# Kernel tuning notes

Hardware: AMD Instinct MI355X
Metric: run time of the kernel (lower is better)

The kernel has to match this reference:

```python
import jax, jax.numpy as jnp
import numpy as np

INPUT, HIDDEN, OUTPUT = 512, 1024, 512
B, T = 256, 512

def setup_inputs() -> dict:
    key = jax.random.key(0)
    ks = jax.random.split(key, 15)
    def lin(k, fin, fout):
        bound = 1.0 / np.sqrt(fin)
        kw, kb = jax.random.split(k)
        W = jax.random.uniform(kw, (fout, fin), jnp.float32, -bound, bound)
        b = jax.random.uniform(kb, (fout,), jnp.float32, -bound, bound)
        return W, b
    x = jax.random.normal(ks[0], (B, T, INPUT), jnp.float32)
    Wxr, bxr = lin(ks[1], INPUT, HIDDEN)
    Whr, bhr = lin(ks[2], HIDDEN, HIDDEN)
    Wxc, bxc = lin(ks[3], INPUT, HIDDEN)
    Whc, bhc = lin(ks[4], HIDDEN, HIDDEN)
    Wxz, bxz = lin(ks[5], INPUT, HIDDEN)
    Whz, bhz = lin(ks[6], HIDDEN, HIDDEN)
    Wo, bo = lin(ks[7], HIDDEN, OUTPUT)
    return {"x": x, "Wxr": Wxr, "bxr": bxr, "Whr": Whr, "bhr": bhr,
            "Wxc": Wxc, "bxc": bxc, "Whc": Whc, "bhc": bhc,
            "Wxz": Wxz, "bxz": bxz, "Whz": Whz, "bhz": bhz,
            "Wo": Wo, "bo": bo}

def reference(x, Wxr, bxr, Whr, bhr, Wxc, bxc, Whc, bhc, Wxz, bxz, Whz, bhz, Wo, bo):
    # Precompute all input-to-gate projections in one big GEMM each: [B,T,H]
    xr = jnp.einsum('bti,hi->bth', x, Wxr) + bxr
    xc = jnp.einsum('bti,hi->bth', x, Wxc) + bxc
    xz = jnp.einsum('bti,hi->bth', x, Wxz) + bxz
    # time-major for scan: [T,B,H]
    xs = (xr.transpose(1, 0, 2), xc.transpose(1, 0, 2), xz.transpose(1, 0, 2))

    h0 = jnp.zeros((x.shape[0], Whr.shape[0]), x.dtype)

    def step(h, xt):
        xr_t, xc_t, xz_t = xt
        r = jax.nn.sigmoid(xr_t + h @ Whr.T + bhr)
        c = jnp.tanh(xc_t + r * (h @ Whc.T + bhc))
        z = jax.nn.sigmoid(xz_t + h @ Whz.T + bhz)
        h_new = (1.0 - z) * h + z * c
        return h_new, None

    h_final, _ = jax.lax.scan(step, h0, xs)
    return h_final @ Wo.T + bo
```

## Files before the change

kernel.cpp:

```cpp
#include <hip/hip_runtime.h>

typedef __attribute__((ext_vector_type(8))) short s16x8;
typedef __attribute__((ext_vector_type(4))) float f32x4;

#define SCOPE_AGENT __HIP_MEMORY_SCOPE_AGENT

static __device__ __forceinline__ unsigned short f2bf(float f) {
    unsigned u = __float_as_uint(f);
    u = (u + 0x7fffu + ((u >> 16) & 1u)) >> 16;
    return (unsigned short)u;
}

static __device__ __forceinline__ unsigned ld_sc1(const unsigned* p) {
    return __hip_atomic_load(p, __ATOMIC_RELAXED, SCOPE_AGENT);
}
static __device__ __forceinline__ void st_sc1(unsigned* p, unsigned v) {
    __hip_atomic_store(p, v, __ATOMIC_RELAXED, SCOPE_AGENT);
}

__global__ void k_cast_bf16(const float* __restrict__ src,
                            unsigned short* __restrict__ dst, int n4) {
    int i = blockIdx.x * blockDim.x + threadIdx.x;
    int stride = gridDim.x * blockDim.x;
    for (; i < n4; i += stride) {
        float4 v = reinterpret_cast<const float4*>(src)[i];
        ushort4 o;
        o.x = f2bf(v.x); o.y = f2bf(v.y); o.z = f2bf(v.z); o.w = f2bf(v.w);
        reinterpret_cast<ushort4*>(dst)[i] = o;
    }
}

__global__ __launch_bounds__(256, 1) void k_gru(
    const unsigned short* __restrict__ x16,
    const unsigned short* __restrict__ wh,
    const unsigned short* __restrict__ wx,
    const unsigned short* __restrict__ wo,
    const float* __restrict__ bxr_, const float* __restrict__ bhr_,
    const float* __restrict__ bxc_, const float* __restrict__ bhc_,
    const float* __restrict__ bxz_, const float* __restrict__ bhz_,
    const float* __restrict__ bo_,
    unsigned short* __restrict__ hring,
    unsigned* __restrict__ slots,
    float* __restrict__ out)
{
    extern __shared__ unsigned short lds[];

    const int tid = threadIdx.x;
    const int bid = blockIdx.x;
    const int xcd = bid & 7;
    const int rb  = xcd >> 1;
    const int jt  = ((bid >> 3) << 1) | (xcd & 1);
    const int b0  = rb * 64;
    const int j0  = jt * 16;

    for (int i = 0; i < 36; ++i) {
        int gidx = i * 256 + tid;
        int rr = gidx / 192;
        int gc = gidx - rr * 192;
        int k  = gc << 3;
        int gate = rr >> 4;
        int j = j0 + (rr & 15);
        const unsigned short* src =
            (k < 1024) ? (wh + ((size_t)gate << 20) + ((size_t)j << 10) + k)
                       : (wx + (size_t)gate * 524288 + ((size_t)j << 9) + (k - 1024));
        s16x8 v = *reinterpret_cast<const s16x8*>(src);
        int boff = ((rr * 192 + gc) << 4) ^ ((rr & 15) << 4);
        *reinterpret_cast<s16x8*>(reinterpret_cast<char*>(lds) + boff) = v;
    }
    __syncthreads();

    const int lane = tid & 63;
    const int wv   = tid >> 6;
    const int l15  = lane & 15;
    const int lk   = lane >> 4;

    const int b   = b0 + wv * 16 + l15;
    const int jq  = j0 + lk * 4;
    const int swz = l15 << 4;
    const int rbase0 = (l15)      * 192 + lk;
    const int rbase1 = (16 + l15) * 192 + lk;
    const int rbase2 = (32 + l15) * 192 + lk;

    float bR[4], bZ[4], bCh[4], bCx[4];
#pragma unroll
    for (int e = 0; e < 4; ++e) {
        int j = jq + e;
        bR[e]  = bxr_[j] + bhr_[j];
        bZ[e]  = bxz_[j] + bhz_[j];
        bCh[e] = bhc_[j];
        bCx[e] = bxc_[j];
    }

    float hreg[4] = {0.f, 0.f, 0.f, 0.f};
    char* lb = reinterpret_cast<char*>(lds);
    const unsigned short* xrowbase = x16 + (size_t)b * 262144 + lk * 8;
    unsigned* myflag  = &slots[(rb << 6) + jt];
    unsigned* gflags  = &slots[rb << 6];

    f32x4 xR = {0.f,0.f,0.f,0.f}, xZ = {0.f,0.f,0.f,0.f}, xC = {0.f,0.f,0.f,0.f};
    {
        s16x8 xf[16];
#pragma unroll
        for (int kk = 0; kk < 16; ++kk)
            xf[kk] = *reinterpret_cast<const s16x8*>(xrowbase + kk * 32);
#pragma unroll
        for (int kk = 0; kk < 16; ++kk) {
            s16x8 w0 = *reinterpret_cast<s16x8*>(lb + (((rbase0 + (kk + 32) * 4) << 4) ^ swz));
            s16x8 w1 = *reinterpret_cast<s16x8*>(lb + (((rbase1 + (kk + 32) * 4) << 4) ^ swz));
            s16x8 w2 = *reinterpret_cast<s16x8*>(lb + (((rbase2 + (kk + 32) * 4) << 4) ^ swz));
            xR = __builtin_amdgcn_mfma_f32_16x16x32_bf16(w0, xf[kk], xR, 0, 0, 0);
            xC = __builtin_amdgcn_mfma_f32_16x16x32_bf16(w1, xf[kk], xC, 0, 0, 0);
            xZ = __builtin_amdgcn_mfma_f32_16x16x32_bf16(w2, xf[kk], xZ, 0, 0, 0);
        }
    }

    for (int t = 0; t < 512; ++t) {
        const unsigned short* hc = hring + (size_t)(t & 7) * 262144;
        unsigned short*       hn = hring + (size_t)((t + 1) & 7) * 262144;

        if (wv == 0) {
            const unsigned tgt = (unsigned)t;
            for (;;) {
                unsigned v = ld_sc1(&gflags[lane]);
                if (__all((int)(v >= tgt))) break;
                __builtin_amdgcn_s_sleep(1);
            }
        }
        if ((t & 7) == 0 && tid == 0)
            (void)__hip_atomic_load(myflag, __ATOMIC_ACQUIRE, SCOPE_AGENT);
        __syncthreads();
        asm volatile("" ::: "memory");

        s16x8 hf[32];
        const unsigned short* hrow = hc + ((size_t)b << 10) + lk * 8;
#pragma unroll
        for (int kk = 0; kk < 32; ++kk)
            hf[kk] = *reinterpret_cast<const s16x8*>(hrow + kk * 32);

        s16x8 xfn[16];
        if (t < 511) {
            const unsigned short* axn = xrowbase + (size_t)(t + 1) * 512;
#pragma unroll
            for (int kk = 0; kk < 16; ++kk)
                xfn[kk] = *reinterpret_cast<const s16x8*>(axn + kk * 32);
        }

        f32x4 aR = xR, aZ = xZ, aCx = xC;
        f32x4 aCh = {0.f,0.f,0.f,0.f};
#pragma unroll
        for (int kk = 0; kk < 32; ++kk) {
            s16x8 w0 = *reinterpret_cast<s16x8*>(lb + (((rbase0 + kk * 4) << 4) ^ swz));
            s16x8 w1 = *reinterpret_cast<s16x8*>(lb + (((rbase1 + kk * 4) << 4) ^ swz));
            s16x8 w2 = *reinterpret_cast<s16x8*>(lb + (((rbase2 + kk * 4) << 4) ^ swz));
            aR  = __builtin_amdgcn_mfma_f32_16x16x32_bf16(w0, hf[kk], aR, 0, 0, 0);
            aCh = __builtin_amdgcn_mfma_f32_16x16x32_bf16(w1, hf[kk], aCh, 0, 0, 0);
            aZ  = __builtin_amdgcn_mfma_f32_16x16x32_bf16(w2, hf[kk], aZ, 0, 0, 0);
        }

        unsigned long long pack = 0ull;
#pragma unroll
        for (int e = 0; e < 4; ++e) {
            float r   = __builtin_amdgcn_rcpf(1.f + __expf(-(aR[e] + bR[e])));
            float zg  = __builtin_amdgcn_rcpf(1.f + __expf(-(aZ[e] + bZ[e])));
            float u2  = aCx[e] + bCx[e] + r * (aCh[e] + bCh[e]);
            float cg  = 1.f - 2.f * __builtin_amdgcn_rcpf(__expf(2.f * u2) + 1.f);
            float hnv = (1.f - zg) * hreg[e] + zg * cg;
            hreg[e] = hnv;
            pack |= (unsigned long long)f2bf(hnv) << (16 * e);
        }
        __hip_atomic_store(
            reinterpret_cast<unsigned long long*>(hn + ((size_t)b << 10) + jq),
            pack, __ATOMIC_RELAXED, SCOPE_AGENT);

        __syncthreads();
        if (tid == 0)
            st_sc1(myflag, (unsigned)(t + 1));

        if (t < 511) {
            xR = {0.f,0.f,0.f,0.f}; xZ = {0.f,0.f,0.f,0.f}; xC = {0.f,0.f,0.f,0.f};
#pragma unroll
            for (int kk = 0; kk < 16; ++kk) {
                s16x8 w0 = *reinterpret_cast<s16x8*>(lb + (((rbase0 + (kk + 32) * 4) << 4) ^ swz));
                s16x8 w1 = *reinterpret_cast<s16x8*>(lb + (((rbase1 + (kk + 32) * 4) << 4) ^ swz));
                s16x8 w2 = *reinterpret_cast<s16x8*>(lb + (((rbase2 + (kk + 32) * 4) << 4) ^ swz));
                xR = __builtin_amdgcn_mfma_f32_16x16x32_bf16(w0, xfn[kk], xR, 0, 0, 0);
                xC = __builtin_amdgcn_mfma_f32_16x16x32_bf16(w1, xfn[kk], xC, 0, 0, 0);
                xZ = __builtin_amdgcn_mfma_f32_16x16x32_bf16(w2, xfn[kk], xZ, 0, 0, 0);
            }
        }
    }

    if (wv == 0) {
        for (;;) {
            unsigned v = ld_sc1(&gflags[lane]);
            if (__all((int)(v >= 512u))) break;
            __builtin_amdgcn_s_sleep(1);
        }
        if (tid == 0)
            (void)__hip_atomic_load(myflag, __ATOMIC_ACQUIRE, SCOPE_AGENT);
    }
    __syncthreads();
    asm volatile("" ::: "memory");

    const unsigned short* hfin = hring;
    const int ocol  = jt * 8 + l15;
    const int ocolc = (l15 < 8) ? ocol : (jt * 8 + 7);
    f32x4 aO = {0.f,0.f,0.f,0.f};
    const unsigned short* hrow = hfin + ((size_t)b << 10) + lk * 8;
    const unsigned short* bw = wo + ((size_t)ocolc << 10) + lk * 8;
#pragma unroll
    for (int kk = 0; kk < 32; ++kk) {
        s16x8 hv = *reinterpret_cast<const s16x8*>(hrow + kk * 32);
        s16x8 wb = *reinterpret_cast<const s16x8*>(bw + kk * 32);
        aO = __builtin_amdgcn_mfma_f32_16x16x32_bf16(hv, wb, aO, 0, 0, 0);
    }
    if (l15 < 8) {
        const float bov = bo_[ocol];
#pragma unroll
        for (int e = 0; e < 4; ++e) {
            out[((size_t)(b0 + wv * 16 + lk * 4 + e) << 9) + ocol] = aO[e] + bov;
        }
    }
}

extern "C" void kernel_launch(void* const* d_in, const int* in_sizes, int n_in,
                              void* d_out, int out_size, void* d_ws, size_t ws_size,
                              hipStream_t stream) {
    const float* x   = (const float*)d_in[0];
    const float* Wxr = (const float*)d_in[1];
    const float* bxr = (const float*)d_in[2];
    const float* Whr = (const float*)d_in[3];
    const float* bhr = (const float*)d_in[4];
    const float* Wxc = (const float*)d_in[5];
    const float* bxc = (const float*)d_in[6];
    const float* Whc = (const float*)d_in[7];
    const float* bhc = (const float*)d_in[8];
    const float* Wxz = (const float*)d_in[9];
    const float* bxz = (const float*)d_in[10];
    const float* Whz = (const float*)d_in[11];
    const float* bhz = (const float*)d_in[12];
    const float* Wo  = (const float*)d_in[13];
    const float* bo  = (const float*)d_in[14];

    char* ws = (char*)d_ws;
    unsigned short* x16  = (unsigned short*)(ws);
    unsigned short* wh   = (unsigned short*)(ws + 134217728);
    unsigned short* wx   = (unsigned short*)(ws + 140509184);
    unsigned short* wo16 = (unsigned short*)(ws + 143654912);
    unsigned short* hring= (unsigned short*)(ws + 144703488);
    unsigned*       slots= (unsigned*)(ws + 148897792);

    auto cast = [&](const float* s, unsigned short* d, int n) {
        int n4 = n >> 2;
        int blocks = (n4 + 255) / 256;
        if (blocks > 4096) blocks = 4096;
        k_cast_bf16<<<blocks, 256, 0, stream>>>(s, d, n4);
    };
    cast(x,   x16, 67108864);
    cast(Whr, wh,            1048576);
    cast(Whc, wh + 1048576,  1048576);
    cast(Whz, wh + 2097152,  1048576);
    cast(Wxr, wx,            524288);
    cast(Wxc, wx + 524288,   524288);
    cast(Wxz, wx + 1048576,  524288);
    cast(Wo,  wo16,          524288);

    hipMemsetAsync(hring, 0, 524288, stream);
    hipMemsetAsync(slots, 0, 1024, stream);

    hipFuncSetAttribute(reinterpret_cast<const void*>(k_gru),
                        hipFuncAttributeMaxDynamicSharedMemorySize, 147456);
    k_gru<<<dim3(256), dim3(256), 147456, stream>>>(
        x16, wh, wx, wo16, bxr, bhr, bxc, bhc, bxz, bhz, bo,
        hring, slots, (float*)d_out);
}
```

Baseline: 3.893 ms.

## Keep Whr and Whz recurrent weights in registers, shrink LDS to Whc plus Wx

The R and Z recurrent weight fragments are loaded once into VGPRs (64 s16x8 per lane), held there with asm barriers, and used directly as MFMA operands. Only the Whc and input-projection weights stay in LDS, which drops dynamic shared memory from 144KB to 80KB and cuts the LDS reads per step by two thirds. The next-step x prefetch also moves after the barrier. The cost is very high register pressure (about 256 extra VGPRs per lane), which risks spills or a forced move to AGPRs.

```diff
diff --git a/kernel.cpp b/kernel.cpp
--- a/kernel.cpp
+++ b/kernel.cpp
@@ -52,20 +52,27 @@
     const int jt  = ((bid >> 3) << 1) | (xcd & 1);
     const int b0  = rb * 64;
     const int j0  = jt * 16;
-
-    for (int i = 0; i < 36; ++i) {
+    char* lb = reinterpret_cast<char*>(lds);
+
+    for (int i = 0; i < 8; ++i) {
         int gidx = i * 256 + tid;
-        int rr = gidx / 192;
-        int gc = gidx - rr * 192;
-        int k  = gc << 3;
+        int rr = gidx >> 7;
+        int gc = gidx & 127;
+        s16x8 v = *reinterpret_cast<const s16x8*>(
+            wh + 1048576 + (size_t)(j0 + rr) * 1024 + gc * 8);
+        int boff = ((rr * 128 + gc) << 4) ^ ((rr & 15) << 4);
+        *reinterpret_cast<s16x8*>(lb + boff) = v;
+    }
+    for (int i = 0; i < 12; ++i) {
+        int gidx = i * 256 + tid;
+        int rr = gidx >> 6;
+        int gc = gidx & 63;
         int gate = rr >> 4;
         int j = j0 + (rr & 15);
-        const unsigned short* src =
-            (k < 1024) ? (wh + ((size_t)gate << 20) + ((size_t)j << 10) + k)
-                       : (wx + (size_t)gate * 524288 + ((size_t)j << 9) + (k - 1024));
-        s16x8 v = *reinterpret_cast<const s16x8*>(src);
-        int boff = ((rr * 192 + gc) << 4) ^ ((rr & 15) << 4);
-        *reinterpret_cast<s16x8*>(reinterpret_cast<char*>(lds) + boff) = v;
+        s16x8 v = *reinterpret_cast<const s16x8*>(
+            wx + (size_t)gate * 524288 + (size_t)j * 512 + gc * 8);
+        int boff = 32768 + (((rr * 64 + gc) << 4) ^ ((rr & 15) << 4));
+        *reinterpret_cast<s16x8*>(lb + boff) = v;
     }
     __syncthreads();
 
@@ -77,9 +84,26 @@
     const int b   = b0 + wv * 16 + l15;
     const int jq  = j0 + lk * 4;
     const int swz = l15 << 4;
-    const int rbase0 = (l15)      * 192 + lk;
-    const int rbase1 = (16 + l15) * 192 + lk;
-    const int rbase2 = (32 + l15) * 192 + lk;
+    const int cbase  = l15 * 128 + lk;
+    const int xbase0 = (l15)      * 64 + lk;
+    const int xbase1 = (16 + l15) * 64 + lk;
+    const int xbase2 = (32 + l15) * 64 + lk;
+
+    s16x8 wr[32], wz[32];
+    {
+        const unsigned short* wrp = wh + (size_t)(j0 + l15) * 1024 + lk * 8;
+        const unsigned short* wzp = wrp + 2097152;
+#pragma unroll
+        for (int kk = 0; kk < 32; ++kk) {
+            wr[kk] = *reinterpret_cast<const s16x8*>(wrp + kk * 32);
+            wz[kk] = *reinterpret_cast<const s16x8*>(wzp + kk * 32);
+        }
+    }
+#pragma unroll
+    for (int kk = 0; kk < 32; ++kk) {
+        asm volatile("" : "+v"(wr[kk]));
+        asm volatile("" : "+v"(wz[kk]));
+    }
 
     float bR[4], bZ[4], bCh[4], bCx[4];
 #pragma unroll
@@ -92,7 +116,6 @@
     }
 
     float hreg[4] = {0.f, 0.f, 0.f, 0.f};
-    char* lb = reinterpret_cast<char*>(lds);
     const unsigned short* xrowbase = x16 + (size_t)b * 262144 + lk * 8;
     unsigned* myflag  = &slots[(rb << 6) + jt];
     unsigned* gflags  = &slots[rb << 6];
@@ -105,9 +128,9 @@
             xf[kk] = *reinterpret_cast<const s16x8*>(xrowbase + kk * 32);
 #pragma unroll
         for (int kk = 0; kk < 16; ++kk) {
-            s16x8 w0 = *reinterpret_cast<s16x8*>(lb + (((rbase0 + (kk + 32) * 4) << 4) ^ swz));
-            s16x8 w1 = *reinterpret_cast<s16x8*>(lb + (((rbase1 + (kk + 32) * 4) << 4) ^ swz));
-            s16x8 w2 = *reinterpret_cast<s16x8*>(lb + (((rbase2 + (kk + 32) * 4) << 4) ^ swz));
+            s16x8 w0 = *reinterpret_cast<s16x8*>(lb + 32768 + (((xbase0 + kk * 4) << 4) ^ swz));
+            s16x8 w1 = *reinterpret_cast<s16x8*>(lb + 32768 + (((xbase1 + kk * 4) << 4) ^ swz));
+            s16x8 w2 = *reinterpret_cast<s16x8*>(lb + 32768 + (((xbase2 + kk * 4) << 4) ^ swz));
             xR = __builtin_amdgcn_mfma_f32_16x16x32_bf16(w0, xf[kk], xR, 0, 0, 0);
             xC = __builtin_amdgcn_mfma_f32_16x16x32_bf16(w1, xf[kk], xC, 0, 0, 0);
             xZ = __builtin_amdgcn_mfma_f32_16x16x32_bf16(w2, xf[kk], xZ, 0, 0, 0);
@@ -137,24 +160,14 @@
         for (int kk = 0; kk < 32; ++kk)
             hf[kk] = *reinterpret_cast<const s16x8*>(hrow + kk * 32);
 
-        s16x8 xfn[16];
-        if (t < 511) {
-            const unsigned short* axn = xrowbase + (size_t)(t + 1) * 512;
-#pragma unroll
-            for (int kk = 0; kk < 16; ++kk)
-                xfn[kk] = *reinterpret_cast<const s16x8*>(axn + kk * 32);
-        }
-
         f32x4 aR = xR, aZ = xZ, aCx = xC;
         f32x4 aCh = {0.f,0.f,0.f,0.f};
 #pragma unroll
         for (int kk = 0; kk < 32; ++kk) {
-            s16x8 w0 = *reinterpret_cast<s16x8*>(lb + (((rbase0 + kk * 4) << 4) ^ swz));
-            s16x8 w1 = *reinterpret_cast<s16x8*>(lb + (((rbase1 + kk * 4) << 4) ^ swz));
-            s16x8 w2 = *reinterpret_cast<s16x8*>(lb + (((rbase2 + kk * 4) << 4) ^ swz));
-            aR  = __builtin_amdgcn_mfma_f32_16x16x32_bf16(w0, hf[kk], aR, 0, 0, 0);
-            aCh = __builtin_amdgcn_mfma_f32_16x16x32_bf16(w1, hf[kk], aCh, 0, 0, 0);
-            aZ  = __builtin_amdgcn_mfma_f32_16x16x32_bf16(w2, hf[kk], aZ, 0, 0, 0);
+            s16x8 w1 = *reinterpret_cast<s16x8*>(lb + (((cbase + kk * 4) << 4) ^ swz));
+            aR  = __builtin_amdgcn_mfma_f32_16x16x32_bf16(wr[kk], hf[kk], aR, 0, 0, 0);
+            aCh = __builtin_amdgcn_mfma_f32_16x16x32_bf16(w1,     hf[kk], aCh, 0, 0, 0);
+            aZ  = __builtin_amdgcn_mfma_f32_16x16x32_bf16(wz[kk], hf[kk], aZ, 0, 0, 0);
         }
 
         unsigned long long pack = 0ull;
@@ -173,16 +186,25 @@
             pack, __ATOMIC_RELAXED, SCOPE_AGENT);
 
         __syncthreads();
-        if (tid == 0)
+
+        s16x8 xfn[16];
+        if (t < 511) {
+            const unsigned short* axn = xrowbase + (size_t)(t + 1) * 512;
+#pragma unroll
+            for (int kk = 0; kk < 16; ++kk)
+                xfn[kk] = *reinterpret_cast<const s16x8*>(axn + kk * 32);
+        }
+        if (tid == 0) {
             st_sc1(myflag, (unsigned)(t + 1));
+        }
 
         if (t < 511) {
             xR = {0.f,0.f,0.f,0.f}; xZ = {0.f,0.f,0.f,0.f}; xC = {0.f,0.f,0.f,0.f};
 #pragma unroll
             for (int kk = 0; kk < 16; ++kk) {
-                s16x8 w0 = *reinterpret_cast<s16x8*>(lb + (((rbase0 + (kk + 32) * 4) << 4) ^ swz));
-                s16x8 w1 = *reinterpret_cast<s16x8*>(lb + (((rbase1 + (kk + 32) * 4) << 4) ^ swz));
-                s16x8 w2 = *reinterpret_cast<s16x8*>(lb + (((rbase2 + (kk + 32) * 4) << 4) ^ swz));
+                s16x8 w0 = *reinterpret_cast<s16x8*>(lb + 32768 + (((xbase0 + kk * 4) << 4) ^ swz));
+                s16x8 w1 = *reinterpret_cast<s16x8*>(lb + 32768 + (((xbase1 + kk * 4) << 4) ^ swz));
+                s16x8 w2 = *reinterpret_cast<s16x8*>(lb + 32768 + (((xbase2 + kk * 4) << 4) ^ swz));
                 xR = __builtin_amdgcn_mfma_f32_16x16x32_bf16(w0, xfn[kk], xR, 0, 0, 0);
                 xC = __builtin_amdgcn_mfma_f32_16x16x32_bf16(w1, xfn[kk], xC, 0, 0, 0);
                 xZ = __builtin_amdgcn_mfma_f32_16x16x32_bf16(w2, xfn[kk], xZ, 0, 0, 0);
@@ -269,8 +291,8 @@
     hipMemsetAsync(slots, 0, 1024, stream);
 
     hipFuncSetAttribute(reinterpret_cast<const void*>(k_gru),
-                        hipFuncAttributeMaxDynamicSharedMemorySize, 147456);
-    k_gru<<<dim3(256), dim3(256), 147456, stream>>>(
+                        hipFuncAttributeMaxDynamicSharedMemorySize, 81920);
+    k_gru<<<dim3(256), dim3(256), 81920, stream>>>(
         x16, wh, wx, wo16, bxr, bhr, bxc, bhc, bxz, bhz, bo,
         hring, slots, (float*)d_out);
 }
```

New measurement: 5.444 ms. 39.8% more time.
